# Kernel optimization log

Hardware: AMD Instinct MI355X
Metric: run time of the kernel (lower is better)

Reference implementation:

```python
import jax, jax.numpy as jnp
import numpy as np

SEQ, D_IN, D_OUT = 4096, 1024, 1024

def setup_inputs() -> dict:
    key = jax.random.key(0)
    k1, k2, k3, k4 = jax.random.split(key, 4)
    return {
        "input": jax.random.normal(k1, (SEQ, D_IN), dtype=jnp.float32),
        "W_query": jax.random.uniform(k2, (D_IN, D_OUT), dtype=jnp.float32),
        "W_key": jax.random.uniform(k3, (D_IN, D_OUT), dtype=jnp.float32),
        "W_value": jax.random.uniform(k4, (D_IN, D_OUT), dtype=jnp.float32),
    }

def reference(input, W_query, W_key, W_value):
    # q, k, v: [S, D_out]
    q = input @ W_query
    k = input @ W_key
    v = input @ W_value
    scale = 1.0 / jnp.sqrt(jnp.asarray(k.shape[-1], dtype=q.dtype))
    scores = (q @ k.T) * scale          # [S, S]
    weights = jax.nn.softmax(scores, axis=-1)
    return weights @ v                  # [S, D_out]
```

## Files before the change

### kernel.cpp

```cpp
#include <hip/hip_runtime.h>
#include <hip/hip_bf16.h>
#include <cstdint>
#include <type_traits>


using u16 = unsigned short;
typedef __attribute__((ext_vector_type(8))) short short8;
typedef __attribute__((ext_vector_type(4))) float floatx4;
typedef __attribute__((ext_vector_type(4))) int intx4;

static constexpr int S_SEQ = 4096;
static constexpr int D_IN  = 1024;
static constexpr int D_OUT = 1024;

__device__ __forceinline__ u16 f2b(float f) {
  uint32_t u = __builtin_bit_cast(uint32_t, f);
  u = (u + 0x7FFFu + ((u >> 16) & 1u)) >> 16;
  return (u16)u;
}
__device__ __forceinline__ float b2f(u16 b) {
  return __builtin_bit_cast(float, (uint32_t)b << 16);
}
__device__ __forceinline__ void load16(const void* g, void* l) {
  __builtin_amdgcn_global_load_lds(
      (const __attribute__((address_space(1))) void*)g,
      (__attribute__((address_space(3))) void*)l,
      16, 0, 0);
}


__global__ void split_bf16_kernel(const float* __restrict__ in,
                                  u16* __restrict__ hi, u16* __restrict__ lo,
                                  int n4) {
  int i = blockIdx.x * blockDim.x + threadIdx.x;
  if (i >= n4) return;
  float4 v = reinterpret_cast<const float4*>(in)[i];
  ushort4 h, l;
  h.x = f2b(v.x); l.x = f2b(v.x - b2f(h.x));
  h.y = f2b(v.y); l.y = f2b(v.y - b2f(h.y));
  h.z = f2b(v.z); l.z = f2b(v.z - b2f(h.z));
  h.w = f2b(v.w); l.w = f2b(v.w - b2f(h.w));
  reinterpret_cast<ushort4*>(hi)[i] = h;
  reinterpret_cast<ushort4*>(lo)[i] = l;
}

__global__ void transpose_w_kernel(const float* __restrict__ Wq,
                                   const float* __restrict__ Wk,
                                   const float* __restrict__ Wv,
                                   u16* __restrict__ WtH, u16* __restrict__ WtL) {
  const int z = blockIdx.z;
  const float* src = (z == 0) ? Wq : (z == 1) ? Wk : Wv;
  u16* dH = WtH + (size_t)z * 1024 * 1024;
  u16* dL = (z < 2) ? WtL + (size_t)z * 1024 * 1024 : nullptr;
  __shared__ float tile[32][33];
  int bx = blockIdx.x * 32, by = blockIdx.y * 32;
  int tx = threadIdx.x, ty = threadIdx.y;
  for (int j = 0; j < 32; j += 8)
    tile[ty + j][tx] = src[(size_t)(by + ty + j) * 1024 + bx + tx];
  __syncthreads();
  for (int j = 0; j < 32; j += 8) {
    float v = tile[tx][ty + j];
    u16 h = f2b(v);
    size_t idx = (size_t)(bx + ty + j) * 1024 + by + tx;
    dH[idx] = h;
    if (dL) dL[idx] = f2b(v - b2f(h));
  }
}

__global__ __launch_bounds__(256)
void qkv_kernel(const u16* __restrict__ Xh, const u16* __restrict__ Xl,
                const u16* __restrict__ WtH, const u16* __restrict__ WtL,
                char* __restrict__ Qa, char* __restrict__ Qb,
                char* __restrict__ Ka, char* __restrict__ Kb,
                u16* __restrict__ Vt) {
  constexpr int BK = 32, K = D_IN;
  constexpr int TILE = 128 * BK;
  __shared__ __align__(16) u16 smem[4 * TILE];
  u16* AsH = smem;
  u16* BsH = smem + TILE;
  u16* AsL = smem + 2 * TILE;
  u16* BsL = smem + 3 * TILE;

  const int tid  = threadIdx.x;
  const int wave = tid >> 6;
  const int lane = tid & 63;
  const int bm   = blockIdx.y * 128;
  const int bn   = blockIdx.x * 128;
  const bool splitB = bn < 2048;
  const int wm   = (wave >> 1) * 64;
  const int wn   = (wave & 1) * 64;
  const int quad = lane >> 4;
  const int l16  = lane & 15;

  const int srow = wave * 16 + (lane >> 2);
  const int scol = (lane & 3) * 8;
  const size_t offA = (size_t)(bm + srow) * K + scol;
  const size_t offB = (size_t)(bn + srow) * K + scol;
  const size_t off64 = (size_t)64 * K;
  const int lds0 = wave * 512;
  const int lds1 = 2048 + wave * 512;

  floatx4 acc[4][4] = {};

  for (int k0 = 0; k0 < K; k0 += BK) {
    __syncthreads();
    load16(Xh + offA + k0,          AsH + lds0);
    load16(Xh + offA + off64 + k0,  AsH + lds1);
    load16(WtH + offB + k0,         BsH + lds0);
    load16(WtH + offB + off64 + k0, BsH + lds1);
    if (splitB) {
      load16(Xl + offA + k0,          AsL + lds0);
      load16(Xl + offA + off64 + k0,  AsL + lds1);
      load16(WtL + offB + k0,         BsL + lds0);
      load16(WtL + offB + off64 + k0, BsL + lds1);
    }
    __syncthreads();

    short8 ah[4], bh[4], al[4], bl[4];
#pragma unroll
    for (int t = 0; t < 4; ++t) {
      ah[t] = *reinterpret_cast<const short8*>(AsH + (wm + t * 16 + l16) * BK + quad * 8);
      bh[t] = *reinterpret_cast<const short8*>(BsH + (wn + t * 16 + l16) * BK + quad * 8);
    }
    if (splitB) {
#pragma unroll
      for (int t = 0; t < 4; ++t) {
        al[t] = *reinterpret_cast<const short8*>(AsL + (wm + t * 16 + l16) * BK + quad * 8);
        bl[t] = *reinterpret_cast<const short8*>(BsL + (wn + t * 16 + l16) * BK + quad * 8);
      }
    }

#pragma unroll
    for (int mt = 0; mt < 4; ++mt)
#pragma unroll
      for (int nt = 0; nt < 4; ++nt)
        acc[mt][nt] = __builtin_amdgcn_mfma_f32_16x16x32_bf16(
            ah[mt], bh[nt], acc[mt][nt], 0, 0, 0);
    if (splitB) {
#pragma unroll
      for (int mt = 0; mt < 4; ++mt)
#pragma unroll
        for (int nt = 0; nt < 4; ++nt) {
          acc[mt][nt] = __builtin_amdgcn_mfma_f32_16x16x32_bf16(
              ah[mt], bl[nt], acc[mt][nt], 0, 0, 0);
          acc[mt][nt] = __builtin_amdgcn_mfma_f32_16x16x32_bf16(
              al[mt], bh[nt], acc[mt][nt], 0, 0, 0);
        }
    }
  }

#pragma unroll
  for (int mt = 0; mt < 4; ++mt) {
#pragma unroll
    for (int nt = 0; nt < 4; ++nt) {
      const int row = bm + wm + mt * 16 + quad * 4;
      const int col = bn + wn + nt * 16 + l16;
      if (bn < 2048) {
        char* Pa = (bn < 1024) ? Qa : Ka;
        char* Pb = (bn < 1024) ? Qb : Kb;
        const int c = (bn < 1024) ? col : col - 1024;
#pragma unroll
        for (int r = 0; r < 4; ++r) {
          float v = acc[mt][nt][r];
          int q16 = (int)rintf(v * 256.f);
          q16 = min(max(q16, -32512), 32512);
          int a = (q16 + 128) >> 8;
          int b = q16 - (a << 8);
          size_t idx = (size_t)(row + r) * 1024 + c;
          Pa[idx] = (char)a;
          Pb[idx] = (char)b;
        }
      } else {
        ushort4 o;
        o.x = f2b(acc[mt][nt][0]);
        o.y = f2b(acc[mt][nt][1]);
        o.z = f2b(acc[mt][nt][2]);
        o.w = f2b(acc[mt][nt][3]);
        *reinterpret_cast<ushort4*>(Vt + (size_t)(col - 2048) * S_SEQ + row) = o;
      }
    }
  }
}

__global__ __launch_bounds__(256)
void s_i8_kernel(const char* __restrict__ Qa, const char* __restrict__ Qb,
                 const char* __restrict__ Ka, const char* __restrict__ Kb,
                 float* __restrict__ S) {
  constexpr int K = D_IN, BK = 128;
  __shared__ __align__(16) char smem[48 * 1024];
  char* QaS = smem;
  char* QbS = smem + 16384;
  char* KaS = smem + 32768;
  char* KbS = smem + 40960;

  const int tid  = threadIdx.x;
  const int wave = tid >> 6;
  const int lane = tid & 63;
  const int bm   = blockIdx.y * 128;
  const int bn   = blockIdx.x * 64;
  const int wm   = (wave >> 1) * 64;
  const int wn   = (wave & 1) * 32;
  const int quad = lane >> 4;
  const int l16  = lane & 15;

  const int srow = lane >> 3;
  const int scol = ((lane & 7) ^ srow) * 16;
  int gQ[4], gK[2];
#pragma unroll
  for (int j = 0; j < 4; ++j)
    gQ[j] = (bm + j * 32 + wave * 8 + srow) * K + scol;
#pragma unroll
  for (int j = 0; j < 2; ++j)
    gK[j] = (bn + j * 32 + wave * 8 + srow) * K + scol;
  const int lQ[4] = {(0 * 32 + wave * 8) * 128, (1 * 32 + wave * 8) * 128,
                     (2 * 32 + wave * 8) * 128, (3 * 32 + wave * 8) * 128};
  const int lK[2] = {(0 * 32 + wave * 8) * 128, (1 * 32 + wave * 8) * 128};

  const int r7 = l16 & 7;
  int cA[4], cB[2];
#pragma unroll
  for (int t = 0; t < 4; ++t)
    cA[t] = (wm + t * 16 + l16) * 128 + ((quad ^ r7) * 16);
#pragma unroll
  for (int t = 0; t < 2; ++t)
    cB[t] = (wn + t * 16 + l16) * 128 + ((quad ^ r7) * 16);

  intx4 accH[4][2] = {};
  intx4 accM[4][2] = {};
  intx4 accL[4][2] = {};

  for (int k0 = 0; k0 < K; k0 += BK) {
    __syncthreads();
#pragma unroll
    for (int j = 0; j < 4; ++j) {
      load16(Qa + gQ[j] + k0, QaS + lQ[j]);
      load16(Qb + gQ[j] + k0, QbS + lQ[j]);
    }
#pragma unroll
    for (int j = 0; j < 2; ++j) {
      load16(Ka + gK[j] + k0, KaS + lK[j]);
      load16(Kb + gK[j] + k0, KbS + lK[j]);
    }
    __syncthreads();

#pragma unroll
    for (int s = 0; s < 2; ++s) {
      const int so = s * 64;
      intx4 ah[4], al[4];
#pragma unroll
      for (int t = 0; t < 4; ++t) {
        ah[t] = *reinterpret_cast<const intx4*>(QaS + (cA[t] ^ so));
        al[t] = *reinterpret_cast<const intx4*>(QbS + (cA[t] ^ so));
      }
#pragma unroll
      for (int nt = 0; nt < 2; ++nt) {
        intx4 bh = *reinterpret_cast<const intx4*>(KaS + (cB[nt] ^ so));
#pragma unroll
        for (int mt = 0; mt < 4; ++mt) {
          accH[mt][nt] = __builtin_amdgcn_mfma_i32_16x16x64_i8(ah[mt], bh, accH[mt][nt], 0, 0, 0);
          accM[mt][nt] = __builtin_amdgcn_mfma_i32_16x16x64_i8(al[mt], bh, accM[mt][nt], 0, 0, 0);
        }
        intx4 bl = *reinterpret_cast<const intx4*>(KbS + (cB[nt] ^ so));
#pragma unroll
        for (int mt = 0; mt < 4; ++mt) {
          accM[mt][nt] = __builtin_amdgcn_mfma_i32_16x16x64_i8(ah[mt], bl, accM[mt][nt], 0, 0, 0);
          accL[mt][nt] = __builtin_amdgcn_mfma_i32_16x16x64_i8(al[mt], bl, accL[mt][nt], 0, 0, 0);
        }
      }
    }
  }

  constexpr float SC = 4.76837158203125e-07f;
#pragma unroll
  for (int mt = 0; mt < 4; ++mt)
#pragma unroll
    for (int nt = 0; nt < 2; ++nt) {
      const int row = bm + wm + mt * 16 + quad * 4;
      const int col = bn + wn + nt * 16 + l16;
#pragma unroll
      for (int r = 0; r < 4; ++r) {
        long long fix = (((long long)accH[mt][nt][r]) << 16) +
                        (((long long)accM[mt][nt][r]) << 8) +
                        (long long)accL[mt][nt][r];
        S[(size_t)(row + r) * S_SEQ + col] = (float)fix * SC;
      }
    }
}

template <bool ATOMIC>
__global__ __launch_bounds__(256)
void gemm_kernel(const u16* __restrict__ A, const u16* __restrict__ Bt,
                 float* __restrict__ C, int M, int N, int K,
                 int lda, int ldb) {
  constexpr int BK = 32;
  constexpr int TILE = 128 * BK;
  __shared__ __align__(16) u16 smem[2 * TILE];
  u16* As = smem;
  u16* Bs = smem + TILE;

  const size_t kof = (size_t)blockIdx.z * K;
  A += kof; Bt += kof;

  const int tid  = threadIdx.x;
  const int wave = tid >> 6;
  const int lane = tid & 63;
  const int bm   = blockIdx.y * 128;
  const int bn   = blockIdx.x * 128;
  const int wm   = (wave >> 1) * 64;
  const int wn   = (wave & 1) * 64;
  const int quad = lane >> 4;
  const int l16  = lane & 15;

  const int srow = wave * 16 + (lane >> 2);
  const int scol = (lane & 3) * 8;
  const size_t offA = (size_t)(bm + srow) * lda + scol;
  const size_t offB = (size_t)(bn + srow) * ldb + scol;
  const size_t offA64 = (size_t)64 * lda;
  const size_t offB64 = (size_t)64 * ldb;
  const int lds0 = wave * 512;
  const int lds1 = 2048 + wave * 512;

  floatx4 acc[4][4] = {};

  for (int k0 = 0; k0 < K; k0 += BK) {
    __syncthreads();
    load16(A + offA + k0,           As + lds0);
    load16(A + offA + offA64 + k0,  As + lds1);
    load16(Bt + offB + k0,          Bs + lds0);
    load16(Bt + offB + offB64 + k0, Bs + lds1);
    __syncthreads();

    short8 af[4], bf[4];
#pragma unroll
    for (int t = 0; t < 4; ++t) {
      af[t] = *reinterpret_cast<const short8*>(As + (wm + t * 16 + l16) * BK + quad * 8);
      bf[t] = *reinterpret_cast<const short8*>(Bs + (wn + t * 16 + l16) * BK + quad * 8);
    }
#pragma unroll
    for (int mt = 0; mt < 4; ++mt)
#pragma unroll
      for (int nt = 0; nt < 4; ++nt)
        acc[mt][nt] = __builtin_amdgcn_mfma_f32_16x16x32_bf16(
            af[mt], bf[nt], acc[mt][nt], 0, 0, 0);
  }

#pragma unroll
  for (int mt = 0; mt < 4; ++mt)
#pragma unroll
    for (int nt = 0; nt < 4; ++nt) {
      const int row = bm + wm + mt * 16 + quad * 4;
      const int col = bn + wn + nt * 16 + l16;
#pragma unroll
      for (int r = 0; r < 4; ++r) {
        if constexpr (ATOMIC)
          atomicAdd(&C[(size_t)(row + r) * N + col], acc[mt][nt][r]);
        else
          C[(size_t)(row + r) * N + col] = acc[mt][nt][r];
      }
    }
}

__global__ __launch_bounds__(256)
void softmax_kernel(const float* __restrict__ S, u16* __restrict__ P) {
  const int row = blockIdx.x, tid = threadIdx.x;
  const int lane = tid & 63, wave = tid >> 6;
  __shared__ float red[4];
  const float4* src = reinterpret_cast<const float4*>(S + (size_t)row * S_SEQ);
  ushort4* dst = reinterpret_cast<ushort4*>(P + (size_t)row * S_SEQ);

  float4 v[4];
  float m = -INFINITY;
#pragma unroll
  for (int t = 0; t < 4; ++t) {
    v[t] = src[tid + t * 256];
    m = fmaxf(m, fmaxf(fmaxf(v[t].x, v[t].y), fmaxf(v[t].z, v[t].w)));
  }
#pragma unroll
  for (int off = 1; off < 64; off <<= 1) m = fmaxf(m, __shfl_xor(m, off));
  if (lane == 0) red[wave] = m;
  __syncthreads();
  m = fmaxf(fmaxf(red[0], red[1]), fmaxf(red[2], red[3]));

  float e[16];
  float l = 0.f;
#pragma unroll
  for (int t = 0; t < 4; ++t) {
    e[4 * t + 0] = __expf(v[t].x - m);
    e[4 * t + 1] = __expf(v[t].y - m);
    e[4 * t + 2] = __expf(v[t].z - m);
    e[4 * t + 3] = __expf(v[t].w - m);
    l += e[4 * t + 0] + e[4 * t + 1] + e[4 * t + 2] + e[4 * t + 3];
  }
#pragma unroll
  for (int off = 1; off < 64; off <<= 1) l += __shfl_xor(l, off);
  __syncthreads();
  if (lane == 0) red[wave] = l;
  __syncthreads();
  const float li = 1.f / (red[0] + red[1] + red[2] + red[3]);

#pragma unroll
  for (int t = 0; t < 4; ++t) {
    ushort4 o;
    o.x = f2b(e[4 * t + 0] * li);
    o.y = f2b(e[4 * t + 1] * li);
    o.z = f2b(e[4 * t + 2] * li);
    o.w = f2b(e[4 * t + 3] * li);
    dst[tid + t * 256] = o;
  }
}


extern "C" void kernel_launch(void* const* d_in, const int* in_sizes, int n_in,
                              void* d_out, int out_size, void* d_ws, size_t ws_size,
                              hipStream_t stream) {
  const float* X  = (const float*)d_in[0];
  const float* Wq = (const float*)d_in[1];
  const float* Wk = (const float*)d_in[2];
  const float* Wv = (const float*)d_in[3];
  float* O = (float*)d_out;
  char* ws = (char*)d_ws;

  const size_t MB = 1u << 20;
  u16*   Xh  = (u16*)(ws);
  u16*   Xl  = (u16*)(ws + 8 * MB);
  u16*   WtH = (u16*)(ws + 16 * MB);
  u16*   WtL = (u16*)(ws + 22 * MB);
  u16*   P   = (u16*)(ws);
  char*  Qa  = (char*)(ws + 32 * MB);
  char*  Qb  = (char*)(ws + 36 * MB);
  char*  Ka  = (char*)(ws + 40 * MB);
  char*  Kb  = (char*)(ws + 44 * MB);
  u16*   Vt  = (u16*)(ws + 64 * MB);
  float* Ss  = (float*)(ws + 72 * MB);

  hipMemsetAsync(O, 0, (size_t)S_SEQ * D_OUT * sizeof(float), stream);

  split_bf16_kernel<<<(S_SEQ * D_IN / 4 + 255) / 256, 256, 0, stream>>>(
      X, Xh, Xl, S_SEQ * D_IN / 4);
  transpose_w_kernel<<<dim3(32, 32, 3), dim3(32, 8), 0, stream>>>(
      Wq, Wk, Wv, WtH, WtL);

  qkv_kernel<<<dim3(3072 / 128, S_SEQ / 128), 256, 0, stream>>>(
      Xh, Xl, WtH, WtL, Qa, Qb, Ka, Kb, Vt);

  s_i8_kernel<<<dim3(S_SEQ / 64, S_SEQ / 128), 256, 0, stream>>>(
      Qa, Qb, Ka, Kb, Ss);

  softmax_kernel<<<S_SEQ, 256, 0, stream>>>(Ss, P);

  gemm_kernel<true><<<dim3(D_OUT / 128, S_SEQ / 128, 2), 256, 0, stream>>>(
      P, Vt, O, S_SEQ, D_OUT, S_SEQ / 2, S_SEQ, S_SEQ);
}
```

Measured before the change: 301.1 us.

## Specialize PV GEMM with BK=64, XOR-swizzled LDS, and split-K of four

Replaces the generic templated GEMM used for P@V with a dedicated kernel. The new kernel loads 64-wide K tiles through an XOR-swizzled LDS layout to avoid bank conflicts, halving the number of barrier pairs per K. It also raises split-K from 2 to 4 and swaps grid axes for better occupancy and locality. The cost is twice as many atomic adds into the output.

After: 309.5 us. +2.8%, slower.

```diff
diff --git a/kernel.cpp b/kernel.cpp
--- a/kernel.cpp
+++ b/kernel.cpp
@@ -287,61 +287,74 @@
     }
 }
 
-template <bool ATOMIC>
 __global__ __launch_bounds__(256)
-void gemm_kernel(const u16* __restrict__ A, const u16* __restrict__ Bt,
-                 float* __restrict__ C, int M, int N, int K,
-                 int lda, int ldb) {
-  constexpr int BK = 32;
-  constexpr int TILE = 128 * BK;
-  __shared__ __align__(16) u16 smem[2 * TILE];
+void pv_kernel(const u16* __restrict__ P, const u16* __restrict__ Vt,
+               float* __restrict__ O) {
+  constexpr int LDA = S_SEQ;
+  constexpr int KS  = S_SEQ / 4;
+  constexpr int BK  = 64;
+  __shared__ __align__(16) u16 smem[2 * 128 * 64];
   u16* As = smem;
-  u16* Bs = smem + TILE;
-
-  const size_t kof = (size_t)blockIdx.z * K;
-  A += kof; Bt += kof;
+  u16* Bs = smem + 128 * 64;
 
   const int tid  = threadIdx.x;
   const int wave = tid >> 6;
   const int lane = tid & 63;
-  const int bm   = blockIdx.y * 128;
-  const int bn   = blockIdx.x * 128;
+  const int bm   = blockIdx.x * 128;
+  const int bn   = blockIdx.y * 128;
+  const int kz   = blockIdx.z * KS;
   const int wm   = (wave >> 1) * 64;
   const int wn   = (wave & 1) * 64;
   const int quad = lane >> 4;
   const int l16  = lane & 15;
 
-  const int srow = wave * 16 + (lane >> 2);
-  const int scol = (lane & 3) * 8;
-  const size_t offA = (size_t)(bm + srow) * lda + scol;
-  const size_t offB = (size_t)(bn + srow) * ldb + scol;
-  const size_t offA64 = (size_t)64 * lda;
-  const size_t offB64 = (size_t)64 * ldb;
-  const int lds0 = wave * 512;
-  const int lds1 = 2048 + wave * 512;
+  const int srow  = lane >> 3;
+  const int selem = ((lane & 7) ^ srow) * 8;
+  size_t gA[4], gB[4];
+#pragma unroll
+  for (int j = 0; j < 4; ++j) {
+    gA[j] = (size_t)(bm + j * 32 + wave * 8 + srow) * LDA + kz + selem;
+    gB[j] = (size_t)(bn + j * 32 + wave * 8 + srow) * LDA + kz + selem;
+  }
+  const int lds[4] = {(wave * 8 + 0) * 64, (wave * 8 + 32) * 64,
+                      (wave * 8 + 64) * 64, (wave * 8 + 96) * 64};
+
+  int cA[4], cB[4];
+#pragma unroll
+  for (int t = 0; t < 4; ++t) {
+    const int Ra = wm + t * 16 + l16;
+    const int Rb = wn + t * 16 + l16;
+    cA[t] = Ra * 64 + ((quad ^ (Ra & 7)) * 8);
+    cB[t] = Rb * 64 + ((quad ^ (Rb & 7)) * 8);
+  }
 
   floatx4 acc[4][4] = {};
 
-  for (int k0 = 0; k0 < K; k0 += BK) {
-    __syncthreads();
-    load16(A + offA + k0,           As + lds0);
-    load16(A + offA + offA64 + k0,  As + lds1);
-    load16(Bt + offB + k0,          Bs + lds0);
-    load16(Bt + offB + offB64 + k0, Bs + lds1);
-    __syncthreads();
-
-    short8 af[4], bf[4];
-#pragma unroll
-    for (int t = 0; t < 4; ++t) {
-      af[t] = *reinterpret_cast<const short8*>(As + (wm + t * 16 + l16) * BK + quad * 8);
-      bf[t] = *reinterpret_cast<const short8*>(Bs + (wn + t * 16 + l16) * BK + quad * 8);
-    }
-#pragma unroll
-    for (int mt = 0; mt < 4; ++mt)
-#pragma unroll
-      for (int nt = 0; nt < 4; ++nt)
-        acc[mt][nt] = __builtin_amdgcn_mfma_f32_16x16x32_bf16(
-            af[mt], bf[nt], acc[mt][nt], 0, 0, 0);
+  for (int k0 = 0; k0 < KS; k0 += BK) {
+    __syncthreads();
+#pragma unroll
+    for (int j = 0; j < 4; ++j) {
+      load16(P + gA[j] + k0,  As + lds[j]);
+      load16(Vt + gB[j] + k0, Bs + lds[j]);
+    }
+    __syncthreads();
+
+#pragma unroll
+    for (int s = 0; s < 2; ++s) {
+      const int so = s * 32;
+      short8 af[4], bf[4];
+#pragma unroll
+      for (int t = 0; t < 4; ++t) {
+        af[t] = *reinterpret_cast<const short8*>(As + (cA[t] ^ so));
+        bf[t] = *reinterpret_cast<const short8*>(Bs + (cB[t] ^ so));
+      }
+#pragma unroll
+      for (int mt = 0; mt < 4; ++mt)
+#pragma unroll
+        for (int nt = 0; nt < 4; ++nt)
+          acc[mt][nt] = __builtin_amdgcn_mfma_f32_16x16x32_bf16(
+              af[mt], bf[nt], acc[mt][nt], 0, 0, 0);
+    }
   }
 
 #pragma unroll
@@ -351,12 +364,8 @@
       const int row = bm + wm + mt * 16 + quad * 4;
       const int col = bn + wn + nt * 16 + l16;
 #pragma unroll
-      for (int r = 0; r < 4; ++r) {
-        if constexpr (ATOMIC)
-          atomicAdd(&C[(size_t)(row + r) * N + col], acc[mt][nt][r]);
-        else
-          C[(size_t)(row + r) * N + col] = acc[mt][nt][r];
-      }
+      for (int r = 0; r < 4; ++r)
+        atomicAdd(&O[(size_t)(row + r) * D_OUT + col], acc[mt][nt][r]);
     }
 }
 
@@ -448,6 +457,5 @@
 
   softmax_kernel<<<S_SEQ, 256, 0, stream>>>(Ss, P);
 
-  gemm_kernel<true><<<dim3(D_OUT / 128, S_SEQ / 128, 2), 256, 0, stream>>>(
-      P, Vt, O, S_SEQ, D_OUT, S_SEQ / 2, S_SEQ, S_SEQ);
-}
+  pv_kernel<<<dim3(S_SEQ / 128, D_OUT / 128, 4), 256, 0, stream>>>(P, Vt, O);
+}
```
